# Performance work log

Measured on AMD Instinct MI355X. Metric: run time of the kernel, lower is better.

The kernel has to match this reference:

```python
import jax, jax.numpy as jnp
import numpy as np

B, S, D = 2, 2048, 1024
H = 16
HD = D // H  # 64


def setup_inputs() -> dict:
    key = jax.random.key(0)
    ks = jax.random.split(key, 7)
    return {
        "query": jax.random.normal(ks[0], (B, S, D), dtype=jnp.float32),
        "sin_q": jax.random.uniform(ks[1], (1, 1, S, HD), dtype=jnp.float32),
        "cos_q": jax.random.uniform(ks[2], (1, 1, S, HD), dtype=jnp.float32),
        "sin_k": jax.random.uniform(ks[3], (1, 1, S, HD), dtype=jnp.float32),
        "cos_k": jax.random.uniform(ks[4], (1, 1, S, HD), dtype=jnp.float32),
        # params: fused QKV proj [D, 3D] (x @ w_in) and output proj [D, D]
        "w_in": jax.random.normal(ks[5], (D, 3 * D), dtype=jnp.float32) / np.sqrt(D),
        "w_out": jax.random.normal(ks[6], (D, D), dtype=jnp.float32) / np.sqrt(D),
    }


def _rotate_half(x):
    x1, x2 = jnp.split(x, 2, axis=-1)
    return jnp.concatenate([-x2, x1], axis=-1)


def _rope(x, sin, cos):
    # prefix = N - sin_len == 0 here, so plain RoPE over the full sequence
    return x * cos + _rotate_half(x) * sin


def reference(query, sin_q, cos_q, sin_k, cos_k, w_in, w_out):
    b, s, d = query.shape
    scale = 1.0 / np.sqrt(HD)
    # fused QKV projection
    qkv = query @ w_in  # [B,S,3D]
    q, k, v = jnp.split(qkv, 3, axis=-1)

    def to_heads(x):
        return x.reshape(b, s, H, HD).transpose(0, 2, 1, 3)  # [B,H,S,HD]

    q, k, v = to_heads(q), to_heads(k), to_heads(v)
    q = _rope(q, sin_q, cos_q)
    k = _rope(k, sin_k, cos_k)
    # causal SDPA
    scores = jnp.einsum("bhqd,bhkd->bhqk", q, k) * scale  # [B,H,S,S]
    causal = jnp.tril(jnp.ones((s, s), dtype=bool))
    scores = jnp.where(causal, scores, jnp.finfo(scores.dtype).min)
    attn = jax.nn.softmax(scores, axis=-1)
    out = jnp.einsum("bhqk,bhkd->bhqd", attn, v)  # [B,H,S,HD]
    out = out.transpose(0, 2, 1, 3).reshape(b, s, d)
    return out @ w_out
```

## Files before the change

### kernel.cpp

```cpp
#include <hip/hip_runtime.h>
#include <hip/hip_bf16.h>
#include <math.h>

#define BB 2
#define SS 2048
#define DD 1024
#define HH 16
#define HDD 64

typedef float f32x4 __attribute__((ext_vector_type(4)));
typedef short s16x8 __attribute__((ext_vector_type(8)));
typedef unsigned short u16x8 __attribute__((ext_vector_type(8)));

__device__ inline unsigned short f2bf(float x) {
  unsigned u = __float_as_uint(x);
  unsigned r = u + 0x7fff + ((u >> 16) & 1);
  return (unsigned short)(r >> 16);
}
__device__ inline float bf2f(unsigned short h) {
  return __uint_as_float(((unsigned)h) << 16);
}

__global__ __launch_bounds__(256) void cast_bf16_kernel(const float* __restrict__ X,
                                                        unsigned short* __restrict__ Xb,
                                                        int n4) {
  int i = blockIdx.x * 256 + threadIdx.x;
  if (i >= n4) return;
  float4 v = ((const float4*)X)[i];
  ushort4 h;
  h.x = f2bf(v.x); h.y = f2bf(v.y); h.z = f2bf(v.z); h.w = f2bf(v.w);
  ((ushort4*)Xb)[i] = h;
}

__global__ __launch_bounds__(256) void split_transpose_kernel(
    const float* __restrict__ W, unsigned short* __restrict__ WTh,
    unsigned short* __restrict__ WTl, int K, int N) {
  __shared__ float tile[64][65];
  const int k0 = blockIdx.y * 64, n0 = blockIdx.x * 64;
  const int t = threadIdx.x;
  const int c = t & 63, rq = t >> 6;
#pragma unroll
  for (int u = 0; u < 16; ++u) {
    int r = u * 4 + rq;
    tile[r][c] = W[(size_t)(k0 + r) * N + n0 + c];
  }
  __syncthreads();
#pragma unroll
  for (int u = 0; u < 16; ++u) {
    int nl = u * 4 + rq;
    float v = tile[c][nl];
    unsigned short h = f2bf(v);
    unsigned short l = f2bf(v - bf2f(h));
    size_t o = (size_t)(n0 + nl) * K + k0 + c;
    WTh[o] = h;
    WTl[o] = l;
  }
}

#define GLDS16(g, l)                                                        \
  __builtin_amdgcn_global_load_lds(                                         \
      (const __attribute__((address_space(1))) unsigned int*)(const void*)(g), \
      (__attribute__((address_space(3))) unsigned int*)(l), 16, 0, 0)

#define GEMM2T_PRE(Ab, BTh, BTl, Kdim)                                      \
  const int t = threadIdx.x;                                                \
  const int bm = blockIdx.y * 128;                                          \
  const int bn = blockIdx.x * 128;                                          \
  const int w = t >> 6, lane = t & 63;                                      \
  const int wrow = (w >> 1) * 64, wcol = (w & 1) * 64;                      \
  const int l15 = lane & 15, l4 = lane >> 4, l7 = lane & 7;                 \
  int ldsoff[4];                                                            \
  const unsigned short* pA[4];                                              \
  const unsigned short* pBh[4];                                             \
  const unsigned short* pBl[4];                                             \
  _Pragma("unroll")                                                         \
  for (int cc = 0; cc < 4; ++cc) {                                          \
    int tp = t + cc * 256;                                                  \
    int srow = tp >> 3;                                                     \
    int gq = (tp & 7) ^ (srow & 7);                                         \
    ldsoff[cc] = tp * 8;                                                    \
    pA[cc]  = (Ab)  + (size_t)(bm + srow) * (Kdim) + gq * 8;                \
    pBh[cc] = (BTh) + (size_t)(bn + srow) * (Kdim) + gq * 8;                \
    pBl[cc] = (BTl) + (size_t)(bn + srow) * (Kdim) + gq * 8;                \
  }                                                                         \
  f32x4 acc[4][4];                                                          \
  const f32x4 z = {0.f, 0.f, 0.f, 0.f};                                     \
  _Pragma("unroll")                                                         \
  for (int m = 0; m < 4; ++m)                                               \
    _Pragma("unroll")                                                       \
    for (int n = 0; n < 4; ++n) acc[m][n] = z;                              \
  for (int k0 = 0; k0 < (Kdim); k0 += 64) {                                 \
    __syncthreads();                                                        \
    _Pragma("unroll")                                                       \
    for (int cc = 0; cc < 4; ++cc) {                                        \
      GLDS16(pA[cc] + k0, &As_b[ldsoff[cc]]);                               \
      GLDS16(pBh[cc] + k0, &Bs_h[ldsoff[cc]]);                              \
      GLDS16(pBl[cc] + k0, &Bs_l[ldsoff[cc]]);                              \
    }                                                                       \
    __syncthreads();                                                        \
    _Pragma("unroll")                                                       \
    for (int ks = 0; ks < 2; ++ks) {                                        \
      const int sw = ((ks * 4 + l4) ^ l7) * 8;                              \
      s16x8 a[4], bh[4], bl[4];                                             \
      _Pragma("unroll")                                                     \
      for (int m = 0; m < 4; ++m)                                           \
        a[m] = *(const s16x8*)&As_b[(wrow + m * 16 + l15) * 64 + sw];       \
      _Pragma("unroll")                                                     \
      for (int n = 0; n < 4; ++n) {                                         \
        int idx = (wcol + n * 16 + l15) * 64 + sw;                          \
        bh[n] = *(const s16x8*)&Bs_h[idx];                                  \
        bl[n] = *(const s16x8*)&Bs_l[idx];                                  \
      }                                                                     \
      _Pragma("unroll")                                                     \
      for (int m = 0; m < 4; ++m)                                           \
        _Pragma("unroll")                                                   \
        for (int n = 0; n < 4; ++n) {                                       \
          acc[m][n] = __builtin_amdgcn_mfma_f32_16x16x32_bf16(a[m], bh[n], acc[m][n], 0, 0, 0); \
          acc[m][n] = __builtin_amdgcn_mfma_f32_16x16x32_bf16(a[m], bl[n], acc[m][n], 0, 0, 0); \
        }                                                                   \
    }                                                                       \
  }

__global__ __launch_bounds__(256) void gemm_qkv_rope_kernel(
    const unsigned short* __restrict__ Ab,
    const unsigned short* __restrict__ BTh, const unsigned short* __restrict__ BTl,
    const float* __restrict__ sin_q, const float* __restrict__ cos_q,
    const float* __restrict__ sin_k, const float* __restrict__ cos_k,
    unsigned short* __restrict__ Qhi, unsigned short* __restrict__ Qlo,
    unsigned short* __restrict__ Khi, unsigned short* __restrict__ Vt) {
  __shared__ __align__(16) unsigned short As_b[128 * 64];
  __shared__ __align__(16) unsigned short Bs_h[128 * 64];
  __shared__ __align__(16) unsigned short Bs_l[128 * 64];
  GEMM2T_PRE(Ab, BTh, BTl, DD)

  const int region = bn >> 10;
  const int hloc = ((bn & 1023) + wcol) >> 6;
  const float QSC = 0.125f * 1.44269504088896340736f;

  if (region == 0) {
#pragma unroll
    for (int m = 0; m < 4; ++m) {
      const int row0 = bm + wrow + m * 16 + l4 * 4;
#pragma unroll
      for (int r = 0; r < 4; ++r) {
        const int row = row0 + r, b = row >> 11, s = row & 2047;
        const size_t ob = ((size_t)(b * HH + hloc) * SS + s) * HDD;
        const float* cq = cos_q + s * HDD;
        const float* sq = sin_q + s * HDD;
#pragma unroll
        for (int np = 0; np < 2; ++np) {
          const int d1 = np * 16 + l15;
          float x1 = acc[m][np][r], x2 = acc[m][np + 2][r];
          float q1 = (x1 * cq[d1] - x2 * sq[d1]) * QSC;
          float q2 = (x2 * cq[d1 + 32] + x1 * sq[d1 + 32]) * QSC;
          unsigned short h1 = f2bf(q1), h2 = f2bf(q2);
          Qhi[ob + d1] = h1;      Qlo[ob + d1] = f2bf(q1 - bf2f(h1));
          Qhi[ob + d1 + 32] = h2; Qlo[ob + d1 + 32] = f2bf(q2 - bf2f(h2));
        }
      }
    }
  } else if (region == 1) {
#pragma unroll
    for (int m = 0; m < 4; ++m) {
      const int row0 = bm + wrow + m * 16 + l4 * 4;
#pragma unroll
      for (int r = 0; r < 4; ++r) {
        const int row = row0 + r, b = row >> 11, s = row & 2047;
        const size_t ob = ((size_t)(b * HH + hloc) * SS + s) * HDD;
        const float* ck = cos_k + s * HDD;
        const float* sk = sin_k + s * HDD;
#pragma unroll
        for (int np = 0; np < 2; ++np) {
          const int d1 = np * 16 + l15;
          float x1 = acc[m][np][r], x2 = acc[m][np + 2][r];
          Khi[ob + d1]      = f2bf(x1 * ck[d1] - x2 * sk[d1]);
          Khi[ob + d1 + 32] = f2bf(x2 * ck[d1 + 32] + x1 * sk[d1 + 32]);
        }
      }
    }
  } else {
#pragma unroll
    for (int m = 0; m < 4; ++m) {
      const int row0 = bm + wrow + m * 16 + l4 * 4;
      const int b = row0 >> 11, s0 = row0 & 2047;
#pragma unroll
      for (int n = 0; n < 4; ++n) {
        const int d = n * 16 + l15;
        ushort4 v4;
        v4.x = f2bf(acc[m][n][0]);
        v4.y = f2bf(acc[m][n][1]);
        v4.z = f2bf(acc[m][n][2]);
        v4.w = f2bf(acc[m][n][3]);
        *(ushort4*)&Vt[((size_t)(b * HH + hloc) * HDD + d) * SS + s0] = v4;
      }
    }
  }
}

__global__ __launch_bounds__(256) void gemm_out_kernel(
    const unsigned short* __restrict__ Ab,
    const unsigned short* __restrict__ BTh, const unsigned short* __restrict__ BTl,
    float* __restrict__ C) {
  __shared__ __align__(16) unsigned short As_b[128 * 64];
  __shared__ __align__(16) unsigned short Bs_h[128 * 64];
  __shared__ __align__(16) unsigned short Bs_l[128 * 64];
  GEMM2T_PRE(Ab, BTh, BTl, DD)

#pragma unroll
  for (int m = 0; m < 4; ++m)
#pragma unroll
    for (int n = 0; n < 4; ++n) {
      f32x4 v = acc[m][n];
      int col = bn + wcol + n * 16 + l15;
      int row0 = bm + wrow + m * 16 + l4 * 4;
#pragma unroll
      for (int r = 0; r < 4; ++r) C[(size_t)(row0 + r) * DD + col] = v[r];
    }
}


#define ATTN_TILE(QH, QL, OO, LS, MM, MASKED, CUR)                               \
  do {                                                                           \
    f32x4 sc[4];                                                                 \
    sc[0] = z; sc[1] = z; sc[2] = z; sc[3] = z;                                  \
    __builtin_amdgcn_s_setprio(1);                                               \
    _Pragma("unroll")                                                            \
    for (int kc = 0; kc < 2; ++kc) {                                             \
      const int swz = ((kc * 4 + l4) ^ l7) * 8;                                  \
      _Pragma("unroll")                                                          \
      for (int n = 0; n < 4; ++n) {                                              \
        const int idx = (n * 16 + l15) * 64 + swz;                               \
        s16x8 kh = *(const s16x8*)&Ks[CUR][idx];                                 \
        sc[n] = __builtin_amdgcn_mfma_f32_16x16x32_bf16(QH[kc], kh, sc[n], 0, 0, 0); \
        sc[n] = __builtin_amdgcn_mfma_f32_16x16x32_bf16(QL[kc], kh, sc[n], 0, 0, 0); \
      }                                                                          \
    }                                                                            \
    __builtin_amdgcn_s_setprio(0);                                               \
    if (MASKED) {                                                                \
      _Pragma("unroll")                                                          \
      for (int n = 0; n < 4; ++n)                                                \
        _Pragma("unroll")                                                        \
        for (int r = 0; r < 4; ++r)                                              \
          if (n * 16 + l15 > w * 16 + l4 * 4 + r) sc[n][r] = -INFINITY;          \
    }                                                                            \
    float pm[4];                                                                 \
    _Pragma("unroll")                                                            \
    for (int r = 0; r < 4; ++r) {                                                \
      float tm = fmaxf(fmaxf(sc[0][r], sc[1][r]), fmaxf(sc[2][r], sc[3][r]));    \
      tm = fmaxf(tm, __shfl_xor(tm, 1));                                         \
      tm = fmaxf(tm, __shfl_xor(tm, 2));                                         \
      tm = fmaxf(tm, __shfl_xor(tm, 4));                                         \
      tm = fmaxf(tm, __shfl_xor(tm, 8));                                         \
      pm[r] = tm;                                                                 \
    }                                                                            \
    float growth = fmaxf(fmaxf(pm[0] - MM[0], pm[1] - MM[1]),                    \
                         fmaxf(pm[2] - MM[2], pm[3] - MM[3]));                   \
    if (!__all(growth <= 8.f)) {                                                 \
      _Pragma("unroll")                                                          \
      for (int r = 0; r < 4; ++r) {                                              \
        float mn = fmaxf(MM[r], pm[r]);                                          \
        float corr = __builtin_amdgcn_exp2f(MM[r] - mn);                         \
        MM[r] = mn;                                                              \
        OO[0][r] *= corr; OO[1][r] *= corr; OO[2][r] *= corr; OO[3][r] *= corr;  \
        LS[r] *= corr;                                                           \
      }                                                                          \
    }                                                                            \
    _Pragma("unroll")                                                            \
    for (int r = 0; r < 4; ++r) {                                                \
      const int pr = (w * 16 + l4 * 4 + r) * 72;                                 \
      _Pragma("unroll")                                                          \
      for (int n = 0; n < 4; ++n)                                                \
        Ps[pr + n * 16 + l15] = f2bf(__builtin_amdgcn_exp2f(sc[n][r] - MM[r]));  \
    }                                                                            \
    const int prow = (w * 16 + l15) * 72;                                        \
    __builtin_amdgcn_s_setprio(1);                                               \
    _Pragma("unroll")                                                            \
    for (int c = 0; c < 2; ++c) {                                                \
      s16x8 pa = *(const s16x8*)&Ps[prow + c * 32 + 8 * l4];                     \
      const int swz = ((c * 4 + l4) ^ l7) * 8;                                   \
      _Pragma("unroll")                                                          \
      for (int n = 0; n < 4; ++n) {                                              \
        s16x8 vb = *(const s16x8*)&Vs[CUR][(n * 16 + l15) * 64 + swz];           \
        OO[n] = __builtin_amdgcn_mfma_f32_16x16x32_bf16(pa, vb, OO[n], 0, 0, 0); \
      }                                                                          \
      LS = __builtin_amdgcn_mfma_f32_16x16x32_bf16(pa, ones, LS, 0, 0, 0);       \
    }                                                                            \
    __builtin_amdgcn_s_setprio(0);                                               \
  } while (0)

#define ATTN_EPI(OO, LS, QI)                                                     \
  do {                                                                           \
    _Pragma("unroll")                                                            \
    for (int r = 0; r < 4; ++r) {                                                \
      const float inv = 1.f / LS[r];                                             \
      const int orow = (QI) * 64 + w * 16 + l4 * 4 + r;                          \
      const size_t ob = ((size_t)b * SS + orow) * DD + h * HDD + l15;            \
      _Pragma("unroll")                                                          \
      for (int n = 0; n < 4; ++n)                                                \
        Ohi[ob + n * 16] = f2bf(OO[n][r] * inv);                                 \
    }                                                                            \
  } while (0)

__global__ __launch_bounds__(256) void attn_mfma_kernel(
    const unsigned short* __restrict__ Qhi, const unsigned short* __restrict__ Qlo,
    const unsigned short* __restrict__ Khi_g, const unsigned short* __restrict__ Vt_g,
    unsigned short* __restrict__ Ohi) {
  __shared__ __align__(16) unsigned short Ks[2][64 * 64];
  __shared__ __align__(16) unsigned short Vs[2][64 * 64];
  __shared__ __align__(16) unsigned short Ps[64 * 72];

  const int t = threadIdx.x;
  const int lane = t & 63;
  const int w = t >> 6;
  const int p = blockIdx.x;
  const int qiA = 31 - p, qiB = p;
  const int bh = blockIdx.y;
  const int b = bh >> 4, h = bh & 15;
  const int l15 = lane & 15, l4 = lane >> 4, l7 = lane & 7;

  s16x8 qhA[2], qlA[2], qhB[2], qlB[2];
  {
    const int rowA = qiA * 64 + w * 16 + l15;
    const unsigned short* qb = Qhi + ((size_t)bh * SS + rowA) * HDD + 8 * l4;
    const unsigned short* qc = Qlo + ((size_t)bh * SS + rowA) * HDD + 8 * l4;
    qhA[0] = *(const s16x8*)(qb);
    qhA[1] = *(const s16x8*)(qb + 32);
    qlA[0] = *(const s16x8*)(qc);
    qlA[1] = *(const s16x8*)(qc + 32);
    const int rowB = qiB * 64 + w * 16 + l15;
    const unsigned short* qd = Qhi + ((size_t)bh * SS + rowB) * HDD + 8 * l4;
    const unsigned short* qe = Qlo + ((size_t)bh * SS + rowB) * HDD + 8 * l4;
    qhB[0] = *(const s16x8*)(qd);
    qhB[1] = *(const s16x8*)(qd + 32);
    qlB[0] = *(const s16x8*)(qe);
    qlB[1] = *(const s16x8*)(qe + 32);
  }

  int lds[2];
  size_t koff[2], voff[2];
#pragma unroll
  for (int c = 0; c < 2; ++c) {
    int G = t + c * 256;
    int row = G >> 3, g = G & 7;
    int gs = g ^ (row & 7);
    lds[c] = G * 8;
    koff[c] = ((size_t)bh * SS + row) * HDD + gs * 8;
    voff[c] = ((size_t)bh * HDD + row) * SS + gs * 8;
  }

  const f32x4 z = {0.f, 0.f, 0.f, 0.f};
  f32x4 oA[4], oB[4], lsA = z, lsB = z;
#pragma unroll
  for (int n = 0; n < 4; ++n) { oA[n] = z; oB[n] = z; }
  float mA[4], mB[4];
#pragma unroll
  for (int r = 0; r < 4; ++r) { mA[r] = -INFINITY; mB[r] = -INFINITY; }

  const short one_bf = (short)0x3F80;
  const s16x8 ones = {one_bf, one_bf, one_bf, one_bf, one_bf, one_bf, one_bf, one_bf};

#pragma unroll
  for (int c = 0; c < 2; ++c) {
    GLDS16(Khi_g + koff[c], &Ks[0][lds[c]]);
    GLDS16(Vt_g + voff[c], &Vs[0][lds[c]]);
  }
  __syncthreads();

  int cur = 0;
  for (int kt = 0; kt <= qiA; ++kt) {
    if (kt < qiA) {
      const size_t ka = (size_t)(kt + 1) * 64 * HDD;
      const size_t va = (size_t)(kt + 1) * 64;
      const int nxt = cur ^ 1;
#pragma unroll
      for (int c = 0; c < 2; ++c) {
        GLDS16(Khi_g + ka + koff[c], &Ks[nxt][lds[c]]);
        GLDS16(Vt_g + va + voff[c], &Vs[nxt][lds[c]]);
      }
    }
    ATTN_TILE(qhA, qlA, oA, lsA, mA, kt == qiA, cur);
    if (kt <= qiB) ATTN_TILE(qhB, qlB, oB, lsB, mB, kt == qiB, cur);
    __syncthreads();
    cur ^= 1;
  }

  ATTN_EPI(oA, lsA, qiA);
  ATTN_EPI(oB, lsB, qiB);
}

extern "C" void kernel_launch(void* const* d_in, const int* in_sizes, int n_in,
                              void* d_out, int out_size, void* d_ws, size_t ws_size,
                              hipStream_t stream) {
  const float* query = (const float*)d_in[0];
  const float* sin_q = (const float*)d_in[1];
  const float* cos_q = (const float*)d_in[2];
  const float* sin_k = (const float*)d_in[3];
  const float* cos_k = (const float*)d_in[4];
  const float* w_in  = (const float*)d_in[5];
  const float* w_out = (const float*)d_in[6];
  float* out = (float*)d_out;

  const int M = BB * SS;
  const size_t MD = (size_t)M * DD;

  unsigned char* ws = (unsigned char*)d_ws;
  size_t off = 0;
  unsigned short* Qb  = (unsigned short*)(ws + off); off += MD * 2;
  unsigned short* B1h = (unsigned short*)(ws + off); off += (size_t)DD * 3 * DD * 2;
  unsigned short* B1l = (unsigned short*)(ws + off); off += (size_t)DD * 3 * DD * 2;
  unsigned short* B2h = (unsigned short*)(ws + off); off += (size_t)DD * DD * 2;
  unsigned short* B2l = (unsigned short*)(ws + off); off += (size_t)DD * DD * 2;
  unsigned short* Qhi = (unsigned short*)(ws + off); off += MD * 2;
  unsigned short* Qlo = (unsigned short*)(ws + off); off += MD * 2;
  unsigned short* Khi = (unsigned short*)(ws + off); off += MD * 2;
  unsigned short* Vt  = (unsigned short*)(ws + off); off += MD * 2;
  unsigned short* Ohi = (unsigned short*)(ws + off); off += MD * 2;

  {
    int n4 = (int)(MD / 4);
    cast_bf16_kernel<<<(n4 + 255) / 256, 256, 0, stream>>>(query, Qb, n4);
    split_transpose_kernel<<<dim3(3 * DD / 64, DD / 64), 256, 0, stream>>>(w_in, B1h, B1l, DD, 3 * DD);
    split_transpose_kernel<<<dim3(DD / 64, DD / 64), 256, 0, stream>>>(w_out, B2h, B2l, DD, DD);
  }
  {
    dim3 grid((3 * DD) / 128, M / 128);
    gemm_qkv_rope_kernel<<<grid, 256, 0, stream>>>(
        Qb, B1h, B1l, sin_q, cos_q, sin_k, cos_k, Qhi, Qlo, Khi, Vt);
  }
  {
    dim3 grid(SS / 128, BB * HH);
    attn_mfma_kernel<<<grid, 256, 0, stream>>>(Qhi, Qlo, Khi, Vt, Ohi);
  }
  {
    dim3 grid(DD / 128, M / 128);
    gemm_out_kernel<<<grid, 256, 0, stream>>>(Ohi, B2h, B2l, out);
  }
}
```

Baseline: 248.3 us.

## Drop low-part weight split in QKV GEMM and remap attention block order

```diff
diff --git a/kernel.cpp b/kernel.cpp
--- a/kernel.cpp
+++ b/kernel.cpp
@@ -13,9 +13,9 @@
 typedef unsigned short u16x8 __attribute__((ext_vector_type(8)));
 
 __device__ inline unsigned short f2bf(float x) {
-  unsigned u = __float_as_uint(x);
-  unsigned r = u + 0x7fff + ((u >> 16) & 1);
-  return (unsigned short)(r >> 16);
+  union { __hip_bfloat16 b; unsigned short u; } cv;
+  cv.b = __float2bfloat16(x);
+  return cv.u;
 }
 __device__ inline float bf2f(unsigned short h) {
   return __uint_as_float(((unsigned)h) << 16);
@@ -32,6 +32,25 @@
   ((ushort4*)Xb)[i] = h;
 }
 
+__global__ __launch_bounds__(256) void cast_transpose_kernel(
+    const float* __restrict__ W, unsigned short* __restrict__ WT, int K, int N) {
+  __shared__ float tile[64][65];
+  const int k0 = blockIdx.y * 64, n0 = blockIdx.x * 64;
+  const int t = threadIdx.x;
+  const int c = t & 63, rq = t >> 6;
+#pragma unroll
+  for (int u = 0; u < 16; ++u) {
+    int r = u * 4 + rq;
+    tile[r][c] = W[(size_t)(k0 + r) * N + n0 + c];
+  }
+  __syncthreads();
+#pragma unroll
+  for (int u = 0; u < 16; ++u) {
+    int nl = u * 4 + rq;
+    WT[(size_t)(n0 + nl) * K + k0 + c] = f2bf(tile[c][nl]);
+  }
+}
+
 __global__ __launch_bounds__(256) void split_transpose_kernel(
     const float* __restrict__ W, unsigned short* __restrict__ WTh,
     unsigned short* __restrict__ WTl, int K, int N) {
@@ -62,7 +81,58 @@
       (const __attribute__((address_space(1))) unsigned int*)(const void*)(g), \
       (__attribute__((address_space(3))) unsigned int*)(l), 16, 0, 0)
 
-#define GEMM2T_PRE(Ab, BTh, BTl, Kdim)                                      \
+#define GEMM1T_PRE(Ab, BTh, Kdim)                                           \
+  const int t = threadIdx.x;                                                \
+  const int bm = blockIdx.y * 128;                                          \
+  const int bn = blockIdx.x * 128;                                          \
+  const int w = t >> 6, lane = t & 63;                                      \
+  const int wrow = (w >> 1) * 64, wcol = (w & 1) * 64;                      \
+  const int l15 = lane & 15, l4 = lane >> 4, l7 = lane & 7;                 \
+  int ldsoff[4];                                                            \
+  const unsigned short* pA[4];                                              \
+  const unsigned short* pBh[4];                                             \
+  _Pragma("unroll")                                                         \
+  for (int cc = 0; cc < 4; ++cc) {                                          \
+    int tp = t + cc * 256;                                                  \
+    int srow = tp >> 3;                                                     \
+    int gq = (tp & 7) ^ (srow & 7);                                         \
+    ldsoff[cc] = tp * 8;                                                    \
+    pA[cc]  = (Ab)  + (size_t)(bm + srow) * (Kdim) + gq * 8;                \
+    pBh[cc] = (BTh) + (size_t)(bn + srow) * (Kdim) + gq * 8;                \
+  }                                                                         \
+  f32x4 acc[4][4];                                                          \
+  const f32x4 z = {0.f, 0.f, 0.f, 0.f};                                     \
+  _Pragma("unroll")                                                         \
+  for (int m = 0; m < 4; ++m)                                               \
+    _Pragma("unroll")                                                       \
+    for (int n = 0; n < 4; ++n) acc[m][n] = z;                              \
+  for (int k0 = 0; k0 < (Kdim); k0 += 64) {                                 \
+    __syncthreads();                                                        \
+    _Pragma("unroll")                                                       \
+    for (int cc = 0; cc < 4; ++cc) {                                        \
+      GLDS16(pA[cc] + k0, &As_b[ldsoff[cc]]);                               \
+      GLDS16(pBh[cc] + k0, &Bs_h[ldsoff[cc]]);                              \
+    }                                                                       \
+    __syncthreads();                                                        \
+    _Pragma("unroll")                                                       \
+    for (int ks = 0; ks < 2; ++ks) {                                        \
+      const int sw = ((ks * 4 + l4) ^ l7) * 8;                              \
+      s16x8 a[4], bh[4];                                                    \
+      _Pragma("unroll")                                                     \
+      for (int m = 0; m < 4; ++m)                                           \
+        a[m] = *(const s16x8*)&As_b[(wrow + m * 16 + l15) * 64 + sw];       \
+      _Pragma("unroll")                                                     \
+      for (int n = 0; n < 4; ++n)                                           \
+        bh[n] = *(const s16x8*)&Bs_h[(wcol + n * 16 + l15) * 64 + sw];      \
+      _Pragma("unroll")                                                     \
+      for (int m = 0; m < 4; ++m)                                           \
+        _Pragma("unroll")                                                   \
+        for (int n = 0; n < 4; ++n)                                         \
+          acc[m][n] = __builtin_amdgcn_mfma_f32_16x16x32_bf16(a[m], bh[n], acc[m][n], 0, 0, 0); \
+    }                                                                       \
+  }
+
+#define GEMM2T_PRE(Ab, BTh, BTl, Kdim)                                     \
   const int t = threadIdx.x;                                                \
   const int bm = blockIdx.y * 128;                                          \
   const int bn = blockIdx.x * 128;                                          \
@@ -123,15 +193,14 @@
 
 __global__ __launch_bounds__(256) void gemm_qkv_rope_kernel(
     const unsigned short* __restrict__ Ab,
-    const unsigned short* __restrict__ BTh, const unsigned short* __restrict__ BTl,
+    const unsigned short* __restrict__ BTh,
     const float* __restrict__ sin_q, const float* __restrict__ cos_q,
     const float* __restrict__ sin_k, const float* __restrict__ cos_k,
     unsigned short* __restrict__ Qhi, unsigned short* __restrict__ Qlo,
     unsigned short* __restrict__ Khi, unsigned short* __restrict__ Vt) {
   __shared__ __align__(16) unsigned short As_b[128 * 64];
   __shared__ __align__(16) unsigned short Bs_h[128 * 64];
-  __shared__ __align__(16) unsigned short Bs_l[128 * 64];
-  GEMM2T_PRE(Ab, BTh, BTl, DD)
+  GEMM1T_PRE(Ab, BTh, DD)
 
   const int region = bn >> 10;
   const int hloc = ((bn & 1023) + wcol) >> 6;
@@ -217,7 +286,6 @@
       for (int r = 0; r < 4; ++r) C[(size_t)(row0 + r) * DD + col] = v[r];
     }
 }
-
 
 #define ATTN_TILE(QH, QL, OO, LS, MM, MASKED, CUR)                               \
   do {                                                                           \
@@ -312,9 +380,10 @@
   const int t = threadIdx.x;
   const int lane = t & 63;
   const int w = t >> 6;
-  const int p = blockIdx.x;
+  const int flat = (int)blockIdx.y * 16 + (int)blockIdx.x;
+  const int p = flat >> 5;
+  const int bh = ((flat & 7) << 2) | ((flat >> 3) & 3);
   const int qiA = 31 - p, qiB = p;
-  const int bh = blockIdx.y;
   const int b = bh >> 4, h = bh & 15;
   const int l15 = lane & 15, l4 = lane >> 4, l7 = lane & 7;
 
@@ -407,7 +476,6 @@
   size_t off = 0;
   unsigned short* Qb  = (unsigned short*)(ws + off); off += MD * 2;
   unsigned short* B1h = (unsigned short*)(ws + off); off += (size_t)DD * 3 * DD * 2;
-  unsigned short* B1l = (unsigned short*)(ws + off); off += (size_t)DD * 3 * DD * 2;
   unsigned short* B2h = (unsigned short*)(ws + off); off += (size_t)DD * DD * 2;
   unsigned short* B2l = (unsigned short*)(ws + off); off += (size_t)DD * DD * 2;
   unsigned short* Qhi = (unsigned short*)(ws + off); off += MD * 2;
@@ -419,13 +487,13 @@
   {
     int n4 = (int)(MD / 4);
     cast_bf16_kernel<<<(n4 + 255) / 256, 256, 0, stream>>>(query, Qb, n4);
-    split_transpose_kernel<<<dim3(3 * DD / 64, DD / 64), 256, 0, stream>>>(w_in, B1h, B1l, DD, 3 * DD);
+    cast_transpose_kernel<<<dim3(3 * DD / 64, DD / 64), 256, 0, stream>>>(w_in, B1h, DD, 3 * DD);
     split_transpose_kernel<<<dim3(DD / 64, DD / 64), 256, 0, stream>>>(w_out, B2h, B2l, DD, DD);
   }
   {
     dim3 grid((3 * DD) / 128, M / 128);
     gemm_qkv_rope_kernel<<<grid, 256, 0, stream>>>(
-        Qb, B1h, B1l, sin_q, cos_q, sin_k, cos_k, Qhi, Qlo, Khi, Vt);
+        Qb, B1h, sin_q, cos_q, sin_k, cos_k, Qhi, Qlo, Khi, Vt);
   }
   {
     dim3 grid(SS / 128, BB * HH);
```

Result: faster. 222.6 us (-10.4%).

## Drop split-bf16 weight correction, one q-tile per attention block with XCD-aware mapping

Applied to the files above, without the earlier changes.

```diff
diff --git a/kernel.cpp b/kernel.cpp
--- a/kernel.cpp
+++ b/kernel.cpp
@@ -13,9 +13,9 @@
 typedef unsigned short u16x8 __attribute__((ext_vector_type(8)));
 
 __device__ inline unsigned short f2bf(float x) {
-  unsigned u = __float_as_uint(x);
-  unsigned r = u + 0x7fff + ((u >> 16) & 1);
-  return (unsigned short)(r >> 16);
+  union { __hip_bfloat16 b; unsigned short u; } cv;
+  cv.b = __float2bfloat16(x);
+  return cv.u;
 }
 __device__ inline float bf2f(unsigned short h) {
   return __uint_as_float(((unsigned)h) << 16);
@@ -32,9 +32,8 @@
   ((ushort4*)Xb)[i] = h;
 }
 
-__global__ __launch_bounds__(256) void split_transpose_kernel(
-    const float* __restrict__ W, unsigned short* __restrict__ WTh,
-    unsigned short* __restrict__ WTl, int K, int N) {
+__global__ __launch_bounds__(256) void cast_transpose_kernel(
+    const float* __restrict__ W, unsigned short* __restrict__ WT, int K, int N) {
   __shared__ float tile[64][65];
   const int k0 = blockIdx.y * 64, n0 = blockIdx.x * 64;
   const int t = threadIdx.x;
@@ -48,12 +47,7 @@
 #pragma unroll
   for (int u = 0; u < 16; ++u) {
     int nl = u * 4 + rq;
-    float v = tile[c][nl];
-    unsigned short h = f2bf(v);
-    unsigned short l = f2bf(v - bf2f(h));
-    size_t o = (size_t)(n0 + nl) * K + k0 + c;
-    WTh[o] = h;
-    WTl[o] = l;
+    WT[(size_t)(n0 + nl) * K + k0 + c] = f2bf(tile[c][nl]);
   }
 }
 
@@ -62,7 +56,7 @@
       (const __attribute__((address_space(1))) unsigned int*)(const void*)(g), \
       (__attribute__((address_space(3))) unsigned int*)(l), 16, 0, 0)
 
-#define GEMM2T_PRE(Ab, BTh, BTl, Kdim)                                      \
+#define GEMM1T_PRE(Ab, BTh, Kdim)                                           \
   const int t = threadIdx.x;                                                \
   const int bm = blockIdx.y * 128;                                          \
   const int bn = blockIdx.x * 128;                                          \
@@ -72,7 +66,6 @@
   int ldsoff[4];                                                            \
   const unsigned short* pA[4];                                              \
   const unsigned short* pBh[4];                                             \
-  const unsigned short* pBl[4];                                             \
   _Pragma("unroll")                                                         \
   for (int cc = 0; cc < 4; ++cc) {                                          \
     int tp = t + cc * 256;                                                  \
@@ -81,7 +74,6 @@
     ldsoff[cc] = tp * 8;                                                    \
     pA[cc]  = (Ab)  + (size_t)(bm + srow) * (Kdim) + gq * 8;                \
     pBh[cc] = (BTh) + (size_t)(bn + srow) * (Kdim) + gq * 8;                \
-    pBl[cc] = (BTl) + (size_t)(bn + srow) * (Kdim) + gq * 8;                \
   }                                                                         \
   f32x4 acc[4][4];                                                          \
   const f32x4 z = {0.f, 0.f, 0.f, 0.f};                                     \
@@ -95,43 +87,36 @@
     for (int cc = 0; cc < 4; ++cc) {                                        \
       GLDS16(pA[cc] + k0, &As_b[ldsoff[cc]]);                               \
       GLDS16(pBh[cc] + k0, &Bs_h[ldsoff[cc]]);                              \
-      GLDS16(pBl[cc] + k0, &Bs_l[ldsoff[cc]]);                              \
     }                                                                       \
     __syncthreads();                                                        \
     _Pragma("unroll")                                                       \
     for (int ks = 0; ks < 2; ++ks) {                                        \
       const int sw = ((ks * 4 + l4) ^ l7) * 8;                              \
-      s16x8 a[4], bh[4], bl[4];                                             \
+      s16x8 a[4], bh[4];                                                    \
       _Pragma("unroll")                                                     \
       for (int m = 0; m < 4; ++m)                                           \
         a[m] = *(const s16x8*)&As_b[(wrow + m * 16 + l15) * 64 + sw];       \
       _Pragma("unroll")                                                     \
-      for (int n = 0; n < 4; ++n) {                                         \
-        int idx = (wcol + n * 16 + l15) * 64 + sw;                          \
-        bh[n] = *(const s16x8*)&Bs_h[idx];                                  \
-        bl[n] = *(const s16x8*)&Bs_l[idx];                                  \
-      }                                                                     \
+      for (int n = 0; n < 4; ++n)                                           \
+        bh[n] = *(const s16x8*)&Bs_h[(wcol + n * 16 + l15) * 64 + sw];      \
       _Pragma("unroll")                                                     \
       for (int m = 0; m < 4; ++m)                                           \
         _Pragma("unroll")                                                   \
-        for (int n = 0; n < 4; ++n) {                                       \
+        for (int n = 0; n < 4; ++n)                                         \
           acc[m][n] = __builtin_amdgcn_mfma_f32_16x16x32_bf16(a[m], bh[n], acc[m][n], 0, 0, 0); \
-          acc[m][n] = __builtin_amdgcn_mfma_f32_16x16x32_bf16(a[m], bl[n], acc[m][n], 0, 0, 0); \
-        }                                                                   \
     }                                                                       \
   }
 
 __global__ __launch_bounds__(256) void gemm_qkv_rope_kernel(
     const unsigned short* __restrict__ Ab,
-    const unsigned short* __restrict__ BTh, const unsigned short* __restrict__ BTl,
+    const unsigned short* __restrict__ BTh,
     const float* __restrict__ sin_q, const float* __restrict__ cos_q,
     const float* __restrict__ sin_k, const float* __restrict__ cos_k,
     unsigned short* __restrict__ Qhi, unsigned short* __restrict__ Qlo,
     unsigned short* __restrict__ Khi, unsigned short* __restrict__ Vt) {
   __shared__ __align__(16) unsigned short As_b[128 * 64];
   __shared__ __align__(16) unsigned short Bs_h[128 * 64];
-  __shared__ __align__(16) unsigned short Bs_l[128 * 64];
-  GEMM2T_PRE(Ab, BTh, BTl, DD)
+  GEMM1T_PRE(Ab, BTh, DD)
 
   const int region = bn >> 10;
   const int hloc = ((bn & 1023) + wcol) >> 6;
@@ -199,12 +184,11 @@
 
 __global__ __launch_bounds__(256) void gemm_out_kernel(
     const unsigned short* __restrict__ Ab,
-    const unsigned short* __restrict__ BTh, const unsigned short* __restrict__ BTl,
+    const unsigned short* __restrict__ BTh,
     float* __restrict__ C) {
   __shared__ __align__(16) unsigned short As_b[128 * 64];
   __shared__ __align__(16) unsigned short Bs_h[128 * 64];
-  __shared__ __align__(16) unsigned short Bs_l[128 * 64];
-  GEMM2T_PRE(Ab, BTh, BTl, DD)
+  GEMM1T_PRE(Ab, BTh, DD)
 
 #pragma unroll
   for (int m = 0; m < 4; ++m)
@@ -288,19 +272,6 @@
     __builtin_amdgcn_s_setprio(0);                                               \
   } while (0)
 
-#define ATTN_EPI(OO, LS, QI)                                                     \
-  do {                                                                           \
-    _Pragma("unroll")                                                            \
-    for (int r = 0; r < 4; ++r) {                                                \
-      const float inv = 1.f / LS[r];                                             \
-      const int orow = (QI) * 64 + w * 16 + l4 * 4 + r;                          \
-      const size_t ob = ((size_t)b * SS + orow) * DD + h * HDD + l15;            \
-      _Pragma("unroll")                                                          \
-      for (int n = 0; n < 4; ++n)                                                \
-        Ohi[ob + n * 16] = f2bf(OO[n][r] * inv);                                 \
-    }                                                                            \
-  } while (0)
-
 __global__ __launch_bounds__(256) void attn_mfma_kernel(
     const unsigned short* __restrict__ Qhi, const unsigned short* __restrict__ Qlo,
     const unsigned short* __restrict__ Khi_g, const unsigned short* __restrict__ Vt_g,
@@ -312,28 +283,22 @@
   const int t = threadIdx.x;
   const int lane = t & 63;
   const int w = t >> 6;
-  const int p = blockIdx.x;
-  const int qiA = 31 - p, qiB = p;
-  const int bh = blockIdx.y;
+  const int flat = (int)blockIdx.y * 32 + (int)blockIdx.x;
+  const int xcd = flat & 7, slot = flat >> 3;
+  const int qi = 31 - (slot >> 2);
+  const int bh = (xcd << 2) | (slot & 3);
   const int b = bh >> 4, h = bh & 15;
   const int l15 = lane & 15, l4 = lane >> 4, l7 = lane & 7;
 
-  s16x8 qhA[2], qlA[2], qhB[2], qlB[2];
+  s16x8 qh[2], ql[2];
   {
-    const int rowA = qiA * 64 + w * 16 + l15;
+    const int rowA = qi * 64 + w * 16 + l15;
     const unsigned short* qb = Qhi + ((size_t)bh * SS + rowA) * HDD + 8 * l4;
     const unsigned short* qc = Qlo + ((size_t)bh * SS + rowA) * HDD + 8 * l4;
-    qhA[0] = *(const s16x8*)(qb);
-    qhA[1] = *(const s16x8*)(qb + 32);
-    qlA[0] = *(const s16x8*)(qc);
-    qlA[1] = *(const s16x8*)(qc + 32);
-    const int rowB = qiB * 64 + w * 16 + l15;
-    const unsigned short* qd = Qhi + ((size_t)bh * SS + rowB) * HDD + 8 * l4;
-    const unsigned short* qe = Qlo + ((size_t)bh * SS + rowB) * HDD + 8 * l4;
-    qhB[0] = *(const s16x8*)(qd);
-    qhB[1] = *(const s16x8*)(qd + 32);
-    qlB[0] = *(const s16x8*)(qe);
-    qlB[1] = *(const s16x8*)(qe + 32);
+    qh[0] = *(const s16x8*)(qb);
+    qh[1] = *(const s16x8*)(qb + 32);
+    ql[0] = *(const s16x8*)(qc);
+    ql[1] = *(const s16x8*)(qc + 32);
   }
 
   int lds[2];
@@ -349,12 +314,12 @@
   }
 
   const f32x4 z = {0.f, 0.f, 0.f, 0.f};
-  f32x4 oA[4], oB[4], lsA = z, lsB = z;
-#pragma unroll
-  for (int n = 0; n < 4; ++n) { oA[n] = z; oB[n] = z; }
-  float mA[4], mB[4];
-#pragma unroll
-  for (int r = 0; r < 4; ++r) { mA[r] = -INFINITY; mB[r] = -INFINITY; }
+  f32x4 o[4], ls = z;
+#pragma unroll
+  for (int n = 0; n < 4; ++n) o[n] = z;
+  float m[4];
+#pragma unroll
+  for (int r = 0; r < 4; ++r) m[r] = -INFINITY;
 
   const short one_bf = (short)0x3F80;
   const s16x8 ones = {one_bf, one_bf, one_bf, one_bf, one_bf, one_bf, one_bf, one_bf};
@@ -367,8 +332,8 @@
   __syncthreads();
 
   int cur = 0;
-  for (int kt = 0; kt <= qiA; ++kt) {
-    if (kt < qiA) {
+  for (int kt = 0; kt <= qi; ++kt) {
+    if (kt < qi) {
       const size_t ka = (size_t)(kt + 1) * 64 * HDD;
       const size_t va = (size_t)(kt + 1) * 64;
       const int nxt = cur ^ 1;
@@ -378,14 +343,20 @@
         GLDS16(Vt_g + va + voff[c], &Vs[nxt][lds[c]]);
       }
     }
-    ATTN_TILE(qhA, qlA, oA, lsA, mA, kt == qiA, cur);
-    if (kt <= qiB) ATTN_TILE(qhB, qlB, oB, lsB, mB, kt == qiB, cur);
+    ATTN_TILE(qh, ql, o, ls, m, kt == qi, cur);
     __syncthreads();
     cur ^= 1;
   }
 
-  ATTN_EPI(oA, lsA, qiA);
-  ATTN_EPI(oB, lsB, qiB);
+#pragma unroll
+  for (int r = 0; r < 4; ++r) {
+    const float inv = 1.f / ls[r];
+    const int orow = qi * 64 + w * 16 + l4 * 4 + r;
+    const size_t ob = ((size_t)b * SS + orow) * DD + h * HDD + l15;
+#pragma unroll
+    for (int n = 0; n < 4; ++n)
+      Ohi[ob + n * 16] = f2bf(o[n][r] * inv);
+  }
 }
 
 extern "C" void kernel_launch(void* const* d_in, const int* in_sizes, int n_in,
@@ -407,9 +378,7 @@
   size_t off = 0;
   unsigned short* Qb  = (unsigned short*)(ws + off); off += MD * 2;
   unsigned short* B1h = (unsigned short*)(ws + off); off += (size_t)DD * 3 * DD * 2;
-  unsigned short* B1l = (unsigned short*)(ws + off); off += (size_t)DD * 3 * DD * 2;
   unsigned short* B2h = (unsigned short*)(ws + off); off += (size_t)DD * DD * 2;
-  unsigned short* B2l = (unsigned short*)(ws + off); off += (size_t)DD * DD * 2;
   unsigned short* Qhi = (unsigned short*)(ws + off); off += MD * 2;
   unsigned short* Qlo = (unsigned short*)(ws + off); off += MD * 2;
   unsigned short* Khi = (unsigned short*)(ws + off); off += MD * 2;
@@ -419,20 +388,20 @@
   {
     int n4 = (int)(MD / 4);
     cast_bf16_kernel<<<(n4 + 255) / 256, 256, 0, stream>>>(query, Qb, n4);
-    split_transpose_kernel<<<dim3(3 * DD / 64, DD / 64), 256, 0, stream>>>(w_in, B1h, B1l, DD, 3 * DD);
-    split_transpose_kernel<<<dim3(DD / 64, DD / 64), 256, 0, stream>>>(w_out, B2h, B2l, DD, DD);
+    cast_transpose_kernel<<<dim3(3 * DD / 64, DD / 64), 256, 0, stream>>>(w_in, B1h, DD, 3 * DD);
+    cast_transpose_kernel<<<dim3(DD / 64, DD / 64), 256, 0, stream>>>(w_out, B2h, DD, DD);
   }
   {
     dim3 grid((3 * DD) / 128, M / 128);
     gemm_qkv_rope_kernel<<<grid, 256, 0, stream>>>(
-        Qb, B1h, B1l, sin_q, cos_q, sin_k, cos_k, Qhi, Qlo, Khi, Vt);
+        Qb, B1h, sin_q, cos_q, sin_k, cos_k, Qhi, Qlo, Khi, Vt);
   }
   {
-    dim3 grid(SS / 128, BB * HH);
+    dim3 grid(32, 32);
     attn_mfma_kernel<<<grid, 256, 0, stream>>>(Qhi, Qlo, Khi, Vt, Ohi);
   }
   {
     dim3 grid(DD / 128, M / 128);
-    gemm_out_kernel<<<grid, 256, 0, stream>>>(Ohi, B2h, B2l, out);
-  }
-}
+    gemm_out_kernel<<<grid, 256, 0, stream>>>(Ohi, B2h, out);
+  }
+}
```

Measured after the change: 209.1 us. 1.19x faster.
